# Performance work log

Hardware: AMD Instinct MI355X
Metric: run time of the kernel (lower is better)

## Reference

```python
import jax, jax.numpy as jnp
import numpy as np


def setup_inputs() -> dict:
    key = jax.random.key(0)
    x = jax.random.normal(key, (4, 5, 256, 32, 32), dtype=jnp.float32)
    return {"x": x, "beta": 1}


def reference(x, beta):
    # x: [B, L, D, H, W] -> [B, L, H, W, D] -> [B, L, N, D], N = H*W
    B, L, D, H, W = x.shape
    xf = jnp.transpose(x, (0, 1, 3, 4, 2)).reshape(B, L, H * W, D)
    # scores: [B, L, N, N]
    scores = jnp.einsum('blnd,blmd->blnm', xf, xf)
    # exp(beta*s)/sum == softmax(beta*s) along last axis (numerically stable form)
    attention = jax.nn.softmax(beta * scores, axis=-1)
    # (x.unsqueeze(2) * attn.unsqueeze(4)).sum(3) == attn @ x
    return jnp.einsum('blnm,blmd->blnd', attention, xf)
```

## Files before the change

kernel.cpp:

```cpp
#include <hip/hip_runtime.h>


typedef __attribute__((ext_vector_type(8))) short bf16x8;
typedef __attribute__((ext_vector_type(4))) float f32x4;
typedef __attribute__((ext_vector_type(16))) float f32x16;

#define GLD16(gp, lp) __builtin_amdgcn_global_load_lds( \
    (const __attribute__((address_space(1))) unsigned int*)(const void*)(gp), \
    (__attribute__((address_space(3))) unsigned int*)(void*)(lp), 16, 0, 0)

#define LDS_BARRIER() __asm__ volatile("s_waitcnt lgkmcnt(0)\ns_barrier" ::: "memory")

__device__ __forceinline__ unsigned int pack_bf16_rne(float a, float b) {
    unsigned int ua = __float_as_uint(a); ua += 0x7FFFu + ((ua >> 16) & 1u);
    unsigned int ub = __float_as_uint(b); ub += 0x7FFFu + ((ub >> 16) & 1u);
    return (ua >> 16) | (ub & 0xFFFF0000u);
}
__device__ __forceinline__ unsigned int pack2_trunc(float lo, float hi) {
    return __builtin_amdgcn_perm(__float_as_uint(hi), __float_as_uint(lo), 0x07060302u);
}

__global__ __launch_bounds__(256) void prep_kernel(const float* __restrict__ x,
                                                   unsigned short* __restrict__ XT) {
    int tid = blockIdx.x * 256 + threadIdx.x;
    int slice = tid >> 12;
    int r = tid & 4095;
    int dcg = r >> 9;
    int n0 = (r & 511) * 2;
    const float* p = x + slice * 262144 + dcg * 32768 + n0;
    float2 L[32];
    #pragma unroll
    for (int j = 0; j < 32; ++j) L[j] = *(const float2*)(p + j * 1024);
    unsigned short* qb = XT + slice * 262144;
    #pragma unroll
    for (int i = 0; i < 2; ++i) {
        int n = n0 + i;
        unsigned short* row = qb + n * 256;
        #pragma unroll
        for (int c = 0; c < 4; ++c) {
            const float2* Lc = &L[c * 8];
            unsigned int w0, w1, w2, w3;
            if (i == 0) {
                w0 = pack_bf16_rne(Lc[0].x, Lc[1].x); w1 = pack_bf16_rne(Lc[2].x, Lc[3].x);
                w2 = pack_bf16_rne(Lc[4].x, Lc[5].x); w3 = pack_bf16_rne(Lc[6].x, Lc[7].x);
            } else {
                w0 = pack_bf16_rne(Lc[0].y, Lc[1].y); w1 = pack_bf16_rne(Lc[2].y, Lc[3].y);
                w2 = pack_bf16_rne(Lc[4].y, Lc[5].y); w3 = pack_bf16_rne(Lc[6].y, Lc[7].y);
            }
            *(uint4*)(row + (((dcg * 4 + c) ^ (n & 7)) * 8)) = make_uint4(w0, w1, w2, w3);
        }
    }
}

__global__ __launch_bounds__(256, 2) void attn_kernel(const unsigned short* __restrict__ XT,
                                                      const float* __restrict__ x,
                                                      const int* __restrict__ beta,
                                                      float* __restrict__ out) {
    __shared__ __align__(16) unsigned short Kmd[64 * 256];
    __shared__ __align__(16) unsigned short Vb[256 * 64];
    __shared__ __align__(16) unsigned short Pb[32 * 64];
    __shared__ float Lpart[4 * 32];
    __shared__ float Ltot[32];

    int bid = blockIdx.x;
    int t = ((bid & 7) * 80) + (bid >> 3);
    int slice = t >> 5, qh = t & 31;

    int tid = threadIdx.x;
    int lane = tid & 63, wv = tid >> 6;
    int nl = lane & 15, g = lane >> 4;
    int lo = lane & 31, hi = lane >> 5;
    int dr = lane >> 4, mq4 = lane & 15;

    const unsigned short* xt_s = XT + slice * 262144;
    const float* xs = x + slice * 262144;
    float cscale = (float)(beta[0]) * 1.44269504089f;

    bf16x8 qf[2][8];
    float mcol[2];
    #pragma unroll
    for (int nq = 0; nq < 2; ++nq) {
        int n = qh * 32 + nq * 16 + nl;
        const unsigned short* qrow = xt_s + n * 256;
        float dg = 0.f;
        #pragma unroll
        for (int ks = 0; ks < 8; ++ks) {
            qf[nq][ks] = *(const bf16x8*)(qrow + (((ks * 4 + g) ^ (n & 7)) * 8));
            const unsigned int* qu = (const unsigned int*)&qf[nq][ks];
            #pragma unroll
            for (int w = 0; w < 4; ++w) {
                float flo = __uint_as_float(qu[w] << 16);
                float fhi = __uint_as_float(qu[w] & 0xFFFF0000u);
                dg = fmaf(flo, flo, dg);
                dg = fmaf(fhi, fhi, dg);
            }
        }
        dg += __shfl_xor(dg, 16);
        dg += __shfl_xor(dg, 32);
        mcol[nq] = dg * cscale;
    }

    f32x16 acc[2];
    acc[0] = (f32x16)(0.f); acc[1] = (f32x16)(0.f);
    float lac0 = 0.f, lac1 = 0.f;

    float4 vreg[16];

    #pragma unroll
    for (int i = 0; i < 16; ++i) {
        int d = wv * 64 + i * 4 + dr;
        vreg[i] = *(const float4*)(xs + d * 1024 + mq4 * 4);
    }
    #pragma unroll
    for (int i = 0; i < 8; ++i) {
        int ch = wv * 8 + i;
        GLD16(xt_s + ch * 512 + lane * 8, &Kmd[ch * 512]);
    }
    #pragma unroll
    for (int i = 0; i < 16; ++i) {
        int d = wv * 64 + i * 4 + dr;
        *(uint2*)(&Vb[d * 64 + (((mq4 >> 1) ^ (d & 7)) * 8) + (mq4 & 1) * 4]) =
            make_uint2(pack2_trunc(vreg[i].x, vreg[i].y), pack2_trunc(vreg[i].z, vreg[i].w));
    }

    for (int kt = 0; kt < 16; ++kt) {
        __syncthreads();

        if (kt < 15) {
            const float* gv = xs + (kt + 1) * 64;
            #pragma unroll
            for (int i = 0; i < 16; ++i) {
                int d = wv * 64 + i * 4 + dr;
                vreg[i] = *(const float4*)(gv + d * 1024 + mq4 * 4);
            }
        }

        f32x4 s0 = {0.f,0.f,0.f,0.f}, s1 = {0.f,0.f,0.f,0.f};
        #pragma unroll
        for (int ks = 0; ks < 8; ++ks) {
            bf16x8 af = *(const bf16x8*)(&Kmd[(wv * 16 + nl) * 256 + (((ks * 4 + g) ^ (nl & 7)) * 8)]);
            s0 = __builtin_amdgcn_mfma_f32_16x16x32_bf16(af, qf[0][ks], s0, 0, 0, 0);
            s1 = __builtin_amdgcn_mfma_f32_16x16x32_bf16(af, qf[1][ks], s1, 0, 0, 0);
        }

        {
            float p0 = exp2f(fmaf(s0[0], cscale, -mcol[0]));
            float p1 = exp2f(fmaf(s0[1], cscale, -mcol[0]));
            float p2 = exp2f(fmaf(s0[2], cscale, -mcol[0]));
            float p3 = exp2f(fmaf(s0[3], cscale, -mcol[0]));
            lac0 += (p0 + p1) + (p2 + p3);
            *(uint2*)(&Pb[nl * 64 + (((wv * 2 + (g >> 1)) ^ (nl & 7)) * 8) + (g & 1) * 4]) =
                make_uint2(pack2_trunc(p0, p1), pack2_trunc(p2, p3));
        }
        {
            float p0 = exp2f(fmaf(s1[0], cscale, -mcol[1]));
            float p1 = exp2f(fmaf(s1[1], cscale, -mcol[1]));
            float p2 = exp2f(fmaf(s1[2], cscale, -mcol[1]));
            float p3 = exp2f(fmaf(s1[3], cscale, -mcol[1]));
            lac1 += (p0 + p1) + (p2 + p3);
            *(uint2*)(&Pb[(16 + nl) * 64 + (((wv * 2 + (g >> 1)) ^ (nl & 7)) * 8) + (g & 1) * 4]) =
                make_uint2(pack2_trunc(p0, p1), pack2_trunc(p2, p3));
        }

        LDS_BARRIER();

        if (kt < 15) {
            const unsigned short* gk = xt_s + (kt + 1) * 16384;
            #pragma unroll
            for (int i = 0; i < 8; ++i) {
                int ch = wv * 8 + i;
                GLD16(gk + ch * 512 + lane * 8, &Kmd[ch * 512]);
            }
        }

        #pragma unroll
        for (int ks = 0; ks < 4; ++ks) {
            bf16x8 pf = *(const bf16x8*)(&Pb[lo * 64 + (((ks * 2 + hi) ^ (lo & 7)) * 8)]);
            #pragma unroll
            for (int db = 0; db < 2; ++db) {
                int d = wv * 64 + db * 32 + lo;
                bf16x8 vf = *(const bf16x8*)(&Vb[d * 64 + (((ks * 2 + hi) ^ (lo & 7)) * 8)]);
                acc[db] = __builtin_amdgcn_mfma_f32_32x32x16_bf16(pf, vf, acc[db], 0, 0, 0);
            }
        }

        LDS_BARRIER();

        if (kt < 15) {
            #pragma unroll
            for (int i = 0; i < 16; ++i) {
                int d = wv * 64 + i * 4 + dr;
                *(uint2*)(&Vb[d * 64 + (((mq4 >> 1) ^ (d & 7)) * 8) + (mq4 & 1) * 4]) =
                    make_uint2(pack2_trunc(vreg[i].x, vreg[i].y), pack2_trunc(vreg[i].z, vreg[i].w));
            }
        }
    }

    lac0 += __shfl_xor(lac0, 16); lac0 += __shfl_xor(lac0, 32);
    lac1 += __shfl_xor(lac1, 16); lac1 += __shfl_xor(lac1, 32);
    if (lane < 16) {
        Lpart[wv * 32 + nl] = lac0;
        Lpart[wv * 32 + 16 + nl] = lac1;
    }
    LDS_BARRIER();
    if (tid < 32)
        Ltot[tid] = 1.f / (Lpart[tid] + Lpart[32 + tid] + Lpart[64 + tid] + Lpart[96 + tid]);
    LDS_BARRIER();

    float* outs = out + slice * 262144 + (qh * 32) * 256;
    #pragma unroll
    for (int rq = 0; rq < 4; ++rq) {
        f32x4 li = *(const f32x4*)(&Ltot[rq * 8 + hi * 4]);
        #pragma unroll
        for (int j = 0; j < 4; ++j) {
            int nloc = rq * 8 + hi * 4 + j;
            #pragma unroll
            for (int db = 0; db < 2; ++db)
                outs[nloc * 256 + wv * 64 + db * 32 + lo] = acc[db][rq * 4 + j] * li[j];
        }
    }
}

extern "C" void kernel_launch(void* const* d_in, const int* in_sizes, int n_in,
                              void* d_out, int out_size, void* d_ws, size_t ws_size,
                              hipStream_t stream) {
    const float* x = (const float*)d_in[0];
    const int* beta = (const int*)d_in[1];
    float* out = (float*)d_out;
    unsigned short* XT = (unsigned short*)d_ws;
    prep_kernel<<<320, 256, 0, stream>>>(x, XT);
    attn_kernel<<<640, 256, 0, stream>>>(XT, x, beta, out);
}
```

Baseline: 142.3 us.

## Pre-pack K and V into MFMA-ready bf16 layouts and load fragments directly to registers

The prep kernel now writes two bf16 copies of the input. One is an unswizzled token-major K layout; the other is a V layout pre-permuted so each lane's MFMA B-fragment is one contiguous 16-byte load. The attention kernel drops the K and V LDS staging and the in-loop fp32-to-bf16 conversion, loading fragments straight from global (L2) into registers. It also double-buffers the P tile so one barrier per iteration suffices and the PV MFMA of one tile overlaps the next S tile. This cuts LDS use to allow three blocks per CU, at the cost of more workspace, more prep-kernel traffic and reliance on L2 for repeated K/V reads.

```diff
diff --git a/kernel.cpp b/kernel.cpp
--- a/kernel.cpp
+++ b/kernel.cpp
@@ -4,10 +4,6 @@
 typedef __attribute__((ext_vector_type(8))) short bf16x8;
 typedef __attribute__((ext_vector_type(4))) float f32x4;
 typedef __attribute__((ext_vector_type(16))) float f32x16;
-
-#define GLD16(gp, lp) __builtin_amdgcn_global_load_lds( \
-    (const __attribute__((address_space(1))) unsigned int*)(const void*)(gp), \
-    (__attribute__((address_space(3))) unsigned int*)(void*)(lp), 16, 0, 0)
 
 #define LDS_BARRIER() __asm__ volatile("s_waitcnt lgkmcnt(0)\ns_barrier" ::: "memory")
 
@@ -21,46 +17,84 @@
 }
 
 __global__ __launch_bounds__(256) void prep_kernel(const float* __restrict__ x,
-                                                   unsigned short* __restrict__ XT) {
-    int tid = blockIdx.x * 256 + threadIdx.x;
-    int slice = tid >> 12;
-    int r = tid & 4095;
-    int dcg = r >> 9;
-    int n0 = (r & 511) * 2;
-    const float* p = x + slice * 262144 + dcg * 32768 + n0;
-    float2 L[32];
-    #pragma unroll
-    for (int j = 0; j < 32; ++j) L[j] = *(const float2*)(p + j * 1024);
-    unsigned short* qb = XT + slice * 262144;
-    #pragma unroll
-    for (int i = 0; i < 2; ++i) {
-        int n = n0 + i;
-        unsigned short* row = qb + n * 256;
-        #pragma unroll
-        for (int c = 0; c < 4; ++c) {
-            const float2* Lc = &L[c * 8];
-            unsigned int w0, w1, w2, w3;
-            if (i == 0) {
-                w0 = pack_bf16_rne(Lc[0].x, Lc[1].x); w1 = pack_bf16_rne(Lc[2].x, Lc[3].x);
-                w2 = pack_bf16_rne(Lc[4].x, Lc[5].x); w3 = pack_bf16_rne(Lc[6].x, Lc[7].x);
-            } else {
-                w0 = pack_bf16_rne(Lc[0].y, Lc[1].y); w1 = pack_bf16_rne(Lc[2].y, Lc[3].y);
-                w2 = pack_bf16_rne(Lc[4].y, Lc[5].y); w3 = pack_bf16_rne(Lc[6].y, Lc[7].y);
+                                                   unsigned short* __restrict__ XT,
+                                                   unsigned short* __restrict__ XV) {
+    __shared__ __align__(16) unsigned char smem[16384];
+    int bid = blockIdx.x;
+    int t = threadIdx.x;
+    if (bid < 640) {
+        uint4* T = (uint4*)smem;
+        int slice = bid >> 5, w = bid & 31;
+        int cc0 = (w & 3) * 32, d0 = (w >> 2) * 32;
+        const float* xs = x + slice * 262144;
+        int ccl = t & 31, dr = t >> 5;
+        #pragma unroll
+        for (int p = 0; p < 4; ++p) {
+            int dl = p * 8 + dr;
+            const float* src = xs + (d0 + dl) * 1024 + (cc0 + ccl) * 8;
+            float4 a = *(const float4*)(src);
+            float4 b = *(const float4*)(src + 4);
+            uint4 o;
+            o.x = pack_bf16_rne(a.x, a.y); o.y = pack_bf16_rne(a.z, a.w);
+            o.z = pack_bf16_rne(b.x, b.y); o.w = pack_bf16_rne(b.z, b.w);
+            T[ccl * 32 + (dl ^ ccl)] = o;
+        }
+        __syncthreads();
+        unsigned short* xv = XV + slice * 262144;
+        int dl2 = t & 31, cr = t >> 5;
+        #pragma unroll
+        for (int p = 0; p < 4; ++p) {
+            int ccl2 = p * 8 + cr;
+            uint4 o = T[ccl2 * 32 + (dl2 ^ ccl2)];
+            *(uint4*)(xv + ((cc0 + ccl2) * 256 + d0 + dl2) * 8) = o;
+        }
+    } else {
+        unsigned long long* TX = (unsigned long long*)smem;
+        int b = bid - 640;
+        int slice = b >> 5, w = b & 31;
+        int d0 = (w & 1) * 128, n0 = (w >> 1) * 64;
+        const float* xs = x + slice * 262144;
+        int nq = t & 15, dqh = t >> 4;
+        #pragma unroll
+        for (int p = 0; p < 2; ++p) {
+            int dq = p * 16 + dqh;
+            const float* src = xs + (d0 + dq * 4) * 1024 + n0 + nq * 4;
+            float4 r0 = *(const float4*)(src);
+            float4 r1 = *(const float4*)(src + 1024);
+            float4 r2 = *(const float4*)(src + 2048);
+            float4 r3 = *(const float4*)(src + 3072);
+            const float* f0 = (const float*)&r0; const float* f1 = (const float*)&r1;
+            const float* f2 = (const float*)&r2; const float* f3 = (const float*)&r3;
+            #pragma unroll
+            for (int j = 0; j < 4; ++j) {
+                int nl2 = nq * 4 + j;
+                unsigned long long q = (unsigned long long)pack_bf16_rne(f0[j], f1[j])
+                    | ((unsigned long long)pack_bf16_rne(f2[j], f3[j]) << 32);
+                TX[nl2 * 32 + (dq ^ (nl2 & 31))] = q;
             }
-            *(uint4*)(row + (((dcg * 4 + c) ^ (n & 7)) * 8)) = make_uint4(w0, w1, w2, w3);
-        }
-    }
-}
-
-__global__ __launch_bounds__(256, 2) void attn_kernel(const unsigned short* __restrict__ XT,
-                                                      const float* __restrict__ x,
+        }
+        __syncthreads();
+        unsigned short* xt = XT + slice * 262144;
+        int ch = t & 15, nr = t >> 4;
+        #pragma unroll
+        for (int p = 0; p < 4; ++p) {
+            int nl2 = p * 16 + nr;
+            unsigned long long qlo = TX[nl2 * 32 + ((ch * 2) ^ (nl2 & 31))];
+            unsigned long long qhi = TX[nl2 * 32 + ((ch * 2 + 1) ^ (nl2 & 31))];
+            uint4 o = make_uint4((unsigned int)qlo, (unsigned int)(qlo >> 32),
+                                 (unsigned int)qhi, (unsigned int)(qhi >> 32));
+            *(uint4*)(xt + (n0 + nl2) * 256 + d0 + ch * 8) = o;
+        }
+    }
+}
+
+__global__ __launch_bounds__(256, 3) void attn_kernel(const unsigned short* __restrict__ XT,
+                                                      const unsigned short* __restrict__ XV,
                                                       const int* __restrict__ beta,
                                                       float* __restrict__ out) {
-    __shared__ __align__(16) unsigned short Kmd[64 * 256];
-    __shared__ __align__(16) unsigned short Vb[256 * 64];
-    __shared__ __align__(16) unsigned short Pb[32 * 64];
+    __shared__ __align__(16) unsigned short Pb[2][32 * 64];
     __shared__ float Lpart[4 * 32];
-    __shared__ float Ltot[32];
+    __shared__ __align__(16) float Ltot[32];
 
     int bid = blockIdx.x;
     int t = ((bid & 7) * 80) + (bid >> 3);
@@ -70,10 +104,9 @@
     int lane = tid & 63, wv = tid >> 6;
     int nl = lane & 15, g = lane >> 4;
     int lo = lane & 31, hi = lane >> 5;
-    int dr = lane >> 4, mq4 = lane & 15;
 
     const unsigned short* xt_s = XT + slice * 262144;
-    const float* xs = x + slice * 262144;
+    const unsigned short* xv_s = XV + slice * 262144;
     float cscale = (float)(beta[0]) * 1.44269504089f;
 
     bf16x8 qf[2][8];
@@ -85,7 +118,7 @@
         float dg = 0.f;
         #pragma unroll
         for (int ks = 0; ks < 8; ++ks) {
-            qf[nq][ks] = *(const bf16x8*)(qrow + (((ks * 4 + g) ^ (n & 7)) * 8));
+            qf[nq][ks] = *(const bf16x8*)(qrow + (ks * 4 + g) * 8);
             const unsigned int* qu = (const unsigned int*)&qf[nq][ks];
             #pragma unroll
             for (int w = 0; w < 4; ++w) {
@@ -104,52 +137,24 @@
     acc[0] = (f32x16)(0.f); acc[1] = (f32x16)(0.f);
     float lac0 = 0.f, lac1 = 0.f;
 
-    float4 vreg[16];
-
-    #pragma unroll
-    for (int i = 0; i < 16; ++i) {
-        int d = wv * 64 + i * 4 + dr;
-        vreg[i] = *(const float4*)(xs + d * 1024 + mq4 * 4);
-    }
-    #pragma unroll
-    for (int i = 0; i < 8; ++i) {
-        int ch = wv * 8 + i;
-        GLD16(xt_s + ch * 512 + lane * 8, &Kmd[ch * 512]);
-    }
-    #pragma unroll
-    for (int i = 0; i < 16; ++i) {
-        int d = wv * 64 + i * 4 + dr;
-        *(uint2*)(&Vb[d * 64 + (((mq4 >> 1) ^ (d & 7)) * 8) + (mq4 & 1) * 4]) =
-            make_uint2(pack2_trunc(vreg[i].x, vreg[i].y), pack2_trunc(vreg[i].z, vreg[i].w));
-    }
-
-    for (int kt = 0; kt < 16; ++kt) {
-        __syncthreads();
-
-        if (kt < 15) {
-            const float* gv = xs + (kt + 1) * 64;
-            #pragma unroll
-            for (int i = 0; i < 16; ++i) {
-                int d = wv * 64 + i * 4 + dr;
-                vreg[i] = *(const float4*)(gv + d * 1024 + mq4 * 4);
-            }
-        }
-
+    bf16x8 af[8], vf[8];
+    const unsigned short* kb = xt_s + (wv * 16 + nl) * 256 + g * 8;
+    const unsigned short* vb = xv_s + (hi * 256 + wv * 64 + lo) * 8;
+
+    auto S_phase = [&](int pbi) {
         f32x4 s0 = {0.f,0.f,0.f,0.f}, s1 = {0.f,0.f,0.f,0.f};
         #pragma unroll
         for (int ks = 0; ks < 8; ++ks) {
-            bf16x8 af = *(const bf16x8*)(&Kmd[(wv * 16 + nl) * 256 + (((ks * 4 + g) ^ (nl & 7)) * 8)]);
-            s0 = __builtin_amdgcn_mfma_f32_16x16x32_bf16(af, qf[0][ks], s0, 0, 0, 0);
-            s1 = __builtin_amdgcn_mfma_f32_16x16x32_bf16(af, qf[1][ks], s1, 0, 0, 0);
-        }
-
+            s0 = __builtin_amdgcn_mfma_f32_16x16x32_bf16(af[ks], qf[0][ks], s0, 0, 0, 0);
+            s1 = __builtin_amdgcn_mfma_f32_16x16x32_bf16(af[ks], qf[1][ks], s1, 0, 0, 0);
+        }
         {
             float p0 = exp2f(fmaf(s0[0], cscale, -mcol[0]));
             float p1 = exp2f(fmaf(s0[1], cscale, -mcol[0]));
             float p2 = exp2f(fmaf(s0[2], cscale, -mcol[0]));
             float p3 = exp2f(fmaf(s0[3], cscale, -mcol[0]));
             lac0 += (p0 + p1) + (p2 + p3);
-            *(uint2*)(&Pb[nl * 64 + (((wv * 2 + (g >> 1)) ^ (nl & 7)) * 8) + (g & 1) * 4]) =
+            *(uint2*)(&Pb[pbi][nl * 64 + (((wv * 2 + (g >> 1)) ^ (nl & 7)) * 8) + (g & 1) * 4]) =
                 make_uint2(pack2_trunc(p0, p1), pack2_trunc(p2, p3));
         }
         {
@@ -158,42 +163,52 @@
             float p2 = exp2f(fmaf(s1[2], cscale, -mcol[1]));
             float p3 = exp2f(fmaf(s1[3], cscale, -mcol[1]));
             lac1 += (p0 + p1) + (p2 + p3);
-            *(uint2*)(&Pb[(16 + nl) * 64 + (((wv * 2 + (g >> 1)) ^ (nl & 7)) * 8) + (g & 1) * 4]) =
+            *(uint2*)(&Pb[pbi][(16 + nl) * 64 + (((wv * 2 + (g >> 1)) ^ (nl & 7)) * 8) + (g & 1) * 4]) =
                 make_uint2(pack2_trunc(p0, p1), pack2_trunc(p2, p3));
         }
-
+    };
+
+    #pragma unroll
+    for (int ks = 0; ks < 8; ++ks) af[ks] = *(const bf16x8*)(kb + ks * 32);
+    #pragma unroll
+    for (int ks = 0; ks < 4; ++ks) {
+        vf[ks * 2]     = *(const bf16x8*)(vb + ks * 4096);
+        vf[ks * 2 + 1] = *(const bf16x8*)(vb + ks * 4096 + 256);
+    }
+    S_phase(0);
+    #pragma unroll
+    for (int ks = 0; ks < 8; ++ks) af[ks] = *(const bf16x8*)(kb + 16384 + ks * 32);
+    LDS_BARRIER();
+
+    for (int kt = 1; kt < 16; ++kt) {
+        int pb = (kt - 1) & 1;
+        #pragma unroll
+        for (int ks = 0; ks < 4; ++ks) {
+            bf16x8 pf = *(const bf16x8*)(&Pb[pb][lo * 64 + (((ks * 2 + hi) ^ (lo & 7)) * 8)]);
+            acc[0] = __builtin_amdgcn_mfma_f32_32x32x16_bf16(pf, vf[ks * 2],     acc[0], 0, 0, 0);
+            acc[1] = __builtin_amdgcn_mfma_f32_32x32x16_bf16(pf, vf[ks * 2 + 1], acc[1], 0, 0, 0);
+        }
+        {
+            const unsigned short* vkt = vb + kt * 16384;
+            #pragma unroll
+            for (int ks = 0; ks < 4; ++ks) {
+                vf[ks * 2]     = *(const bf16x8*)(vkt + ks * 4096);
+                vf[ks * 2 + 1] = *(const bf16x8*)(vkt + ks * 4096 + 256);
+            }
+        }
+        S_phase(kt & 1);
+        if (kt < 15) {
+            const unsigned short* kkt = kb + (kt + 1) * 16384;
+            #pragma unroll
+            for (int ks = 0; ks < 8; ++ks) af[ks] = *(const bf16x8*)(kkt + ks * 32);
+        }
         LDS_BARRIER();
-
-        if (kt < 15) {
-            const unsigned short* gk = xt_s + (kt + 1) * 16384;
-            #pragma unroll
-            for (int i = 0; i < 8; ++i) {
-                int ch = wv * 8 + i;
-                GLD16(gk + ch * 512 + lane * 8, &Kmd[ch * 512]);
-            }
-        }
-
-        #pragma unroll
-        for (int ks = 0; ks < 4; ++ks) {
-            bf16x8 pf = *(const bf16x8*)(&Pb[lo * 64 + (((ks * 2 + hi) ^ (lo & 7)) * 8)]);
-            #pragma unroll
-            for (int db = 0; db < 2; ++db) {
-                int d = wv * 64 + db * 32 + lo;
-                bf16x8 vf = *(const bf16x8*)(&Vb[d * 64 + (((ks * 2 + hi) ^ (lo & 7)) * 8)]);
-                acc[db] = __builtin_amdgcn_mfma_f32_32x32x16_bf16(pf, vf, acc[db], 0, 0, 0);
-            }
-        }
-
-        LDS_BARRIER();
-
-        if (kt < 15) {
-            #pragma unroll
-            for (int i = 0; i < 16; ++i) {
-                int d = wv * 64 + i * 4 + dr;
-                *(uint2*)(&Vb[d * 64 + (((mq4 >> 1) ^ (d & 7)) * 8) + (mq4 & 1) * 4]) =
-                    make_uint2(pack2_trunc(vreg[i].x, vreg[i].y), pack2_trunc(vreg[i].z, vreg[i].w));
-            }
-        }
+    }
+    #pragma unroll
+    for (int ks = 0; ks < 4; ++ks) {
+        bf16x8 pf = *(const bf16x8*)(&Pb[1][lo * 64 + (((ks * 2 + hi) ^ (lo & 7)) * 8)]);
+        acc[0] = __builtin_amdgcn_mfma_f32_32x32x16_bf16(pf, vf[ks * 2],     acc[0], 0, 0, 0);
+        acc[1] = __builtin_amdgcn_mfma_f32_32x32x16_bf16(pf, vf[ks * 2 + 1], acc[1], 0, 0, 0);
     }
 
     lac0 += __shfl_xor(lac0, 16); lac0 += __shfl_xor(lac0, 32);
@@ -228,6 +243,7 @@
     const int* beta = (const int*)d_in[1];
     float* out = (float*)d_out;
     unsigned short* XT = (unsigned short*)d_ws;
-    prep_kernel<<<320, 256, 0, stream>>>(x, XT);
-    attn_kernel<<<640, 256, 0, stream>>>(XT, x, beta, out);
-}
+    unsigned short* XV = (unsigned short*)d_ws + 5242880;
+    prep_kernel<<<1280, 256, 0, stream>>>(x, XT, XV);
+    attn_kernel<<<640, 256, 0, stream>>>(XT, XV, beta, out);
+}
```

Measured after the change: 195.9 us. 1.38x slower.
